# Kernel optimization log

Measured on AMD Instinct MI355X. Metric: run time of the kernel, lower is better.

## Reference

```python
import jax, jax.numpy as jnp
import numpy as np

DIM = 128
HEADS = 4
OUT = DIM // HEADS  # 32
NEG_SLOPE = 0.2
EPS = 1e-16


def setup_inputs() -> dict:
    key = jax.random.key(0)
    k1, k2, k3, k4, k5, k6 = jax.random.split(key, 6)
    B, T, E = 4, 4096, 131072
    x = jax.random.normal(k1, (B, T, DIM), dtype=jnp.float32)
    edge_index = jax.random.randint(k2, (2, E), 0, T, dtype=jnp.int64)
    # GATConv params (PyG layout): lin weight [heads*out, in], att [heads, out], bias [heads*out]
    W = jax.random.normal(k3, (HEADS * OUT, DIM), dtype=jnp.float32) / np.sqrt(DIM)
    att_src = jax.random.normal(k4, (HEADS, OUT), dtype=jnp.float32) / np.sqrt(OUT)
    att_dst = jax.random.normal(k5, (HEADS, OUT), dtype=jnp.float32) / np.sqrt(OUT)
    bias = jax.random.normal(k6, (HEADS * OUT,), dtype=jnp.float32) * 0.01
    return {"x": x, "edge_index": edge_index, "W": W, "att_src": att_src, "att_dst": att_dst, "bias": bias}


def reference(x, edge_index, W, att_src, att_dst, bias):
    B, T, D = x.shape
    N = B * T
    E = edge_index.shape[1]
    # batch the temporal edge list: repeat(1, B) + per-graph node offset b*T
    offsets = jnp.repeat(jnp.arange(B, dtype=edge_index.dtype) * T, E)
    src = jnp.tile(edge_index[0], B) + offsets
    dst = jnp.tile(edge_index[1], B) + offsets
    # PyG GATConv default add_self_loops=True
    loops = jnp.arange(N, dtype=edge_index.dtype)
    src = jnp.concatenate([src, loops])
    dst = jnp.concatenate([dst, loops])

    h = (x.reshape(N, D) @ W.T).reshape(N, HEADS, OUT)          # [N,H,O]
    a_src = jnp.einsum('nho,ho->nh', h, att_src)                # [N,H]
    a_dst = jnp.einsum('nho,ho->nh', h, att_dst)

    e = a_src[src] + a_dst[dst]                                  # [Etot,H]
    e = jax.nn.leaky_relu(e, NEG_SLOPE)
    # segment softmax over destination neighborhoods
    m = jax.ops.segment_max(e, dst, num_segments=N)              # [N,H]
    ex = jnp.exp(e - m[dst])
    s = jax.ops.segment_sum(ex, dst, num_segments=N)
    alpha = ex / (s[dst] + EPS)                                  # [Etot,H]

    msg = h[src] * alpha[:, :, None]                             # [Etot,H,O]
    out = jax.ops.segment_sum(msg, dst, num_segments=N)          # [N,H,O]
    out = out.reshape(N, HEADS * OUT) + bias
    return out.reshape(B, T, D)
```

## Files before the change

kernel.cpp:

```cpp
#include <hip/hip_runtime.h>

#define TPG   4096
#define NHEAD 4
#define DIMD  128
#define NEG   0.2f

__device__ __forceinline__ int load_edge(const void* ei, int is64, long idx) {
  if (is64) return (int)((const long long*)ei)[idx];
  return ((const int*)ei)[idx];
}

__device__ __forceinline__ int detect64_block(const unsigned* __restrict__ ei) {
  __shared__ int s64;
  int t = threadIdx.x;
  if (t == 0) s64 = 1;
  __syncthreads();
  if (t < 256) {
    unsigned v = ei[2 * t + 1];
    if (v != 0u) s64 = 0;
  }
  __syncthreads();
  return s64;
}

__global__ __launch_bounds__(256) void k_gemm(
    const float* __restrict__ x, const float* __restrict__ W,
    const float* __restrict__ atts, const float* __restrict__ attd,
    float* __restrict__ h, float* __restrict__ as_n, float* __restrict__ ad_n,
    int* __restrict__ counts, int* __restrict__ done) {
  __shared__ float4 xs4[16][33];
  int t = threadIdx.x;
  if (blockIdx.x < 16) counts[(blockIdx.x << 8) + t] = 0;
  if (blockIdx.x == 16 && t == 0) *done = 0;
  int base = blockIdx.x * 16;
  const float4* x4 = (const float4*)x;
  for (int i = t; i < 512; i += 256) {
    xs4[i >> 5][i & 31] = x4[base * 32 + i];
  }
  __syncthreads();

  int n_sub = t & 15, cgrp = t >> 4;
  int c0 = cgrp * 8;
  const float4* W4 = (const float4*)W;
  float acc[8];
#pragma unroll
  for (int k = 0; k < 8; ++k) acc[k] = 0.f;

  for (int db = 0; db < 32; db += 8) {
    float4 xa[8];
#pragma unroll
    for (int i = 0; i < 8; ++i) xa[i] = xs4[n_sub][db + i];
#pragma unroll
    for (int k = 0; k < 8; ++k) {
      const float4* wr = W4 + (c0 + k) * 32 + db;
      float a = acc[k];
#pragma unroll
      for (int i = 0; i < 8; ++i) {
        float4 w = wr[i];
        a = fmaf(xa[i].x, w.x, a);
        a = fmaf(xa[i].y, w.y, a);
        a = fmaf(xa[i].z, w.z, a);
        a = fmaf(xa[i].w, w.w, a);
      }
      acc[k] = a;
    }
  }

  int n = base + n_sub;
  float4* hp = (float4*)(h + ((size_t)n << 7) + c0);
  hp[0] = make_float4(acc[0], acc[1], acc[2], acc[3]);
  hp[1] = make_float4(acc[4], acc[5], acc[6], acc[7]);

  float ps = 0.f, pd = 0.f;
#pragma unroll
  for (int k = 0; k < 8; ++k) {
    ps = fmaf(acc[k], atts[c0 + k], ps);
    pd = fmaf(acc[k], attd[c0 + k], pd);
  }
  ps += __shfl_xor(ps, 16); ps += __shfl_xor(ps, 32);
  pd += __shfl_xor(pd, 16); pd += __shfl_xor(pd, 32);
  if ((t & 48) == 0) {
    as_n[(n << 2) + (t >> 6)] = ps;
    ad_n[(n << 2) + (t >> 6)] = pd;
  }
}

__global__ __launch_bounds__(256) void k_histscan(
    const void* __restrict__ ei, int* __restrict__ counts,
    int* __restrict__ offs, int* __restrict__ cursor,
    int* __restrict__ done, int E) {
  int is64 = detect64_block((const unsigned*)ei);
  int t = threadIdx.x;
  int e = blockIdx.x * 256 + t;
  if (e < E) {
    int dst = load_edge(ei, is64, (long)E + e);
    atomicAdd(&counts[dst], 1);
  }
  __syncthreads();
  __shared__ int lastFlag;
  if (t == 0) {
    __threadfence();
    int prev = atomicAdd(done, 1);
    lastFlag = (prev == (int)gridDim.x - 1);
  }
  __syncthreads();
  if (!lastFlag) return;

  int v[16]; int sum = 0;
#pragma unroll
  for (int i = 0; i < 16; ++i) { v[i] = atomicAdd(&counts[t * 16 + i], 0); sum += v[i]; }
  int lane = t & 63, w = t >> 6;
  int sc = sum;
#pragma unroll
  for (int off = 1; off < 64; off <<= 1) {
    int o = __shfl_up(sc, off);
    if (lane >= off) sc += o;
  }
  __shared__ int wsum[4];
  if (lane == 63) wsum[w] = sc;
  __syncthreads();
  int wo = 0;
  for (int i = 0; i < w; ++i) wo += wsum[i];
  int a = wo + sc - sum;
#pragma unroll
  for (int i = 0; i < 16; ++i) {
    offs[t * 16 + i] = a; cursor[t * 16 + i] = a; a += v[i];
  }
  if (t == 255) offs[4096] = a;
}

__global__ __launch_bounds__(256) void k_scatter(const void* __restrict__ ei,
                                                 int* __restrict__ cursor,
                                                 int* __restrict__ esrc, int E) {
  int is64 = detect64_block((const unsigned*)ei);
  int e = blockIdx.x * blockDim.x + threadIdx.x;
  if (e >= E) return;
  int src = load_edge(ei, is64, e);
  int dst = load_edge(ei, is64, (long)E + e);
  int pos = atomicAdd(&cursor[dst], 1);
  esrc[pos] = src;
}

__global__ __launch_bounds__(256) void k_aggr(
    const int* __restrict__ offs, const int* __restrict__ esrc,
    const float* __restrict__ h, const float* __restrict__ as_n,
    const float* __restrict__ ad_n, const float* __restrict__ bias,
    float* __restrict__ out) {
  int bid = blockIdx.x;
  int wv = threadIdx.x >> 6;
  int lane = threadIdx.x & 63;
  int xcd = bid & 7, slot = bid >> 3;
  int g = xcd >> 1, pair = xcd & 1;
  int group = (slot << 1) + pair;
  int n = (g << 12) + (group << 1) + (wv >> 1);
  n = __builtin_amdgcn_readfirstlane(n);
  int hpair = wv & 1;
  int tloc = n & (TPG - 1);
  int nodebase = n - tloc;
  int beg = __builtin_amdgcn_readfirstlane(offs[tloc]);
  int end = __builtin_amdgcn_readfirstlane(offs[tloc + 1]);

  int hh = (hpair << 1) + (lane >> 5);
  int ch = (hh << 5) + (lane & 31);
  float adst = ad_n[(n << 2) + hh];

  float m, s, acc;
  {
    float e = as_n[(n << 2) + hh] + adst;
    e = e > 0.f ? e : NEG * e;
    m = e; s = 1.f;
    acc = h[((size_t)n << 7) + ch];
  }

  for (int j0 = beg; j0 < end; j0 += 8) {
    int sgk[8];
#pragma unroll
    for (int k = 0; k < 8; ++k) {
      int j = j0 + k;
      sgk[k] = (j < end) ? (nodebase + esrc[j]) : n;
    }
    float hv[8];
#pragma unroll
    for (int k = 0; k < 8; ++k) hv[k] = h[((size_t)sgk[k] << 7) + ch];
    float ek[8];
#pragma unroll
    for (int k = 0; k < 8; ++k) {
      float e = as_n[(sgk[k] << 2) + hh] + adst;
      e = e > 0.f ? e : NEG * e;
      ek[k] = (j0 + k < end) ? e : -1e30f;
    }
    float bm = fmaxf(fmaxf(fmaxf(ek[0], ek[1]), fmaxf(ek[2], ek[3])),
                     fmaxf(fmaxf(ek[4], ek[5]), fmaxf(ek[6], ek[7])));
    float mn = fmaxf(m, bm);
    float r = __expf(m - mn);
    float ps = 0.f, pa = 0.f;
#pragma unroll
    for (int k = 0; k < 8; ++k) {
      float al = __expf(ek[k] - mn);
      ps += al;
      pa = fmaf(al, hv[k], pa);
    }
    acc = fmaf(acc, r, pa);
    s = fmaf(s, r, ps);
    m = mn;
  }

  float invs = 1.f / (s + 1e-16f);
  out[((size_t)n << 7) + ch] = fmaf(acc, invs, bias[ch]);
}

extern "C" void kernel_launch(void* const* d_in, const int* in_sizes, int n_in,
                              void* d_out, int out_size, void* d_ws, size_t ws_size,
                              hipStream_t stream) {
  const float* x    = (const float*)d_in[0];
  const void*  ei   = d_in[1];
  const float* W    = (const float*)d_in[2];
  const float* atts = (const float*)d_in[3];
  const float* attd = (const float*)d_in[4];
  const float* bias = (const float*)d_in[5];
  float* out = (float*)d_out;

  int N = in_sizes[0] / DIMD;
  int E = in_sizes[1] / 2;

  char* p = (char*)d_ws;
  float* h      = (float*)p; p += (size_t)N * DIMD * 4;
  float* as_n   = (float*)p; p += (size_t)N * NHEAD * 4;
  float* ad_n   = (float*)p; p += (size_t)N * NHEAD * 4;
  int*   counts = (int*)p;   p += (size_t)TPG * 4;
  int*   offs   = (int*)p;   p += (size_t)(TPG + 1) * 4;
  int*   cursor = (int*)p;   p += (size_t)TPG * 4;
  int*   esrc   = (int*)p;   p += (size_t)E * 4;
  int*   done   = (int*)p;   p += 4;

  k_gemm<<<N / 16, 256, 0, stream>>>(x, W, atts, attd, h, as_n, ad_n, counts, done);
  k_histscan<<<(E + 255) / 256, 256, 0, stream>>>(ei, counts, offs, cursor, done, E);
  k_scatter<<<(E + 255) / 256, 256, 0, stream>>>(ei, cursor, esrc, E);
  k_aggr<<<N / 2, 256, 0, stream>>>(offs, esrc, h, as_n, ad_n, bias, out);
}
```

Before: 170.6 us.

## Process one node per wave with float2 loads and double-buffered edge gathers

The aggregation kernel now assigns a whole wave to one destination node, with each lane handling two channels through float2 loads. It drops the XCD-aware node remapping and halves the grid. The edge loop is software-pipelined with two register buffers, so the next batch's indices and feature gathers are issued before the current batch's softmax math. This aims to hide gather latency and halve per-edge index and score loads, at the cost of more registers and a separate tail path for the leftover edges.

```diff
diff --git a/kernel.cpp b/kernel.cpp
--- a/kernel.cpp
+++ b/kernel.cpp
@@ -4,6 +4,7 @@
 #define NHEAD 4
 #define DIMD  128
 #define NEG   0.2f
+#define BSZ   8
 
 __device__ __forceinline__ int load_edge(const void* ei, int is64, long idx) {
   if (is64) return (int)((const long long*)ei)[idx];
@@ -141,72 +142,125 @@
   esrc[pos] = src;
 }
 
+#define IDX(sg, t)                                                        \
+  { _Pragma("unroll") for (int k = 0; k < BSZ; ++k)                       \
+      sg[k] = nodebase + esrc[beg + ((t) << 3) + k]; }
+
+#define VLD(sg, as, hv)                                                   \
+  { _Pragma("unroll") for (int k = 0; k < BSZ; ++k)                       \
+      as[k] = as_n[(sg[k] << 2) + myh];                                   \
+    _Pragma("unroll") for (int k = 0; k < BSZ; ++k)                       \
+      hv[k] = h2[((size_t)sg[k] << 6) + lane]; }
+
+#define MATH(as, hv)                                                      \
+  { float ek[BSZ];                                                        \
+    _Pragma("unroll") for (int k = 0; k < BSZ; ++k) {                     \
+      float e = as[k] + adst; ek[k] = e > 0.f ? e : NEG * e; }            \
+    float bm = ek[0];                                                     \
+    _Pragma("unroll") for (int k = 1; k < BSZ; ++k) bm = fmaxf(bm, ek[k]);\
+    float mn = fmaxf(m, bm);                                              \
+    float r = __expf(m - mn);                                             \
+    float ps = 0.f, px = 0.f, py = 0.f;                                   \
+    _Pragma("unroll") for (int k = 0; k < BSZ; ++k) {                     \
+      float al = __expf(ek[k] - mn);                                      \
+      ps += al;                                                           \
+      px = fmaf(al, hv[k].x, px);                                         \
+      py = fmaf(al, hv[k].y, py);                                         \
+    }                                                                     \
+    acc.x = fmaf(acc.x, r, px);                                           \
+    acc.y = fmaf(acc.y, r, py);                                           \
+    s = fmaf(s, r, ps);                                                   \
+    m = mn; }
+
 __global__ __launch_bounds__(256) void k_aggr(
     const int* __restrict__ offs, const int* __restrict__ esrc,
     const float* __restrict__ h, const float* __restrict__ as_n,
     const float* __restrict__ ad_n, const float* __restrict__ bias,
     float* __restrict__ out) {
-  int bid = blockIdx.x;
-  int wv = threadIdx.x >> 6;
   int lane = threadIdx.x & 63;
-  int xcd = bid & 7, slot = bid >> 3;
-  int g = xcd >> 1, pair = xcd & 1;
-  int group = (slot << 1) + pair;
-  int n = (g << 12) + (group << 1) + (wv >> 1);
-  n = __builtin_amdgcn_readfirstlane(n);
-  int hpair = wv & 1;
+  int n = __builtin_amdgcn_readfirstlane((blockIdx.x << 2) + (threadIdx.x >> 6));
   int tloc = n & (TPG - 1);
   int nodebase = n - tloc;
   int beg = __builtin_amdgcn_readfirstlane(offs[tloc]);
   int end = __builtin_amdgcn_readfirstlane(offs[tloc + 1]);
 
-  int hh = (hpair << 1) + (lane >> 5);
-  int ch = (hh << 5) + (lane & 31);
-  float adst = ad_n[(n << 2) + hh];
-
-  float m, s, acc;
+  int myh = lane >> 4;
+  const float2* __restrict__ h2 = (const float2*)h;
+  float adst = ad_n[(n << 2) + myh];
+
+  float m, s;
+  float2 acc;
   {
-    float e = as_n[(n << 2) + hh] + adst;
+    float e = as_n[(n << 2) + myh] + adst;
     e = e > 0.f ? e : NEG * e;
     m = e; s = 1.f;
-    acc = h[((size_t)n << 7) + ch];
-  }
-
-  for (int j0 = beg; j0 < end; j0 += 8) {
-    int sgk[8];
-#pragma unroll
-    for (int k = 0; k < 8; ++k) {
-      int j = j0 + k;
-      sgk[k] = (j < end) ? (nodebase + esrc[j]) : n;
-    }
-    float hv[8];
-#pragma unroll
-    for (int k = 0; k < 8; ++k) hv[k] = h[((size_t)sgk[k] << 7) + ch];
-    float ek[8];
-#pragma unroll
-    for (int k = 0; k < 8; ++k) {
-      float e = as_n[(sgk[k] << 2) + hh] + adst;
-      e = e > 0.f ? e : NEG * e;
-      ek[k] = (j0 + k < end) ? e : -1e30f;
-    }
-    float bm = fmaxf(fmaxf(fmaxf(ek[0], ek[1]), fmaxf(ek[2], ek[3])),
-                     fmaxf(fmaxf(ek[4], ek[5]), fmaxf(ek[6], ek[7])));
+    acc = h2[((size_t)n << 6) + lane];
+  }
+
+  int F = (end - beg) >> 3;
+  int sgA[BSZ], sgB[BSZ];
+  float asA[BSZ], asB[BSZ];
+  float2 hvA[BSZ], hvB[BSZ];
+
+  if (F > 0) { IDX(sgA, 0); VLD(sgA, asA, hvA); }
+  if (F > 1) { IDX(sgB, 1); }
+  int t = 0;
+  while (t < F) {
+    if (t + 1 < F) VLD(sgB, asB, hvB);
+    if (t + 2 < F) IDX(sgA, t + 2);
+    MATH(asA, hvA);
+    ++t; if (t >= F) break;
+    if (t + 1 < F) VLD(sgA, asA, hvA);
+    if (t + 2 < F) IDX(sgB, t + 2);
+    MATH(asB, hvB);
+    ++t;
+  }
+
+  int jt = beg + (F << 3);
+  if (jt < end) {
+    int sg[BSZ];
+#pragma unroll
+    for (int k = 0; k < BSZ; ++k) {
+      int j = jt + k;
+      sg[k] = (j < end) ? (nodebase + esrc[j]) : n;
+    }
+    float as_[BSZ]; float2 hv[BSZ];
+#pragma unroll
+    for (int k = 0; k < BSZ; ++k) as_[k] = as_n[(sg[k] << 2) + myh];
+#pragma unroll
+    for (int k = 0; k < BSZ; ++k) hv[k] = h2[((size_t)sg[k] << 6) + lane];
+    float ek[BSZ];
+#pragma unroll
+    for (int k = 0; k < BSZ; ++k) {
+      float e = as_[k] + adst; e = e > 0.f ? e : NEG * e;
+      ek[k] = (jt + k < end) ? e : -1e30f;
+    }
+    float bm = ek[0];
+#pragma unroll
+    for (int k = 1; k < BSZ; ++k) bm = fmaxf(bm, ek[k]);
     float mn = fmaxf(m, bm);
     float r = __expf(m - mn);
-    float ps = 0.f, pa = 0.f;
-#pragma unroll
-    for (int k = 0; k < 8; ++k) {
+    float ps = 0.f, px = 0.f, py = 0.f;
+#pragma unroll
+    for (int k = 0; k < BSZ; ++k) {
       float al = __expf(ek[k] - mn);
       ps += al;
-      pa = fmaf(al, hv[k], pa);
-    }
-    acc = fmaf(acc, r, pa);
+      px = fmaf(al, hv[k].x, px);
+      py = fmaf(al, hv[k].y, py);
+    }
+    acc.x = fmaf(acc.x, r, px);
+    acc.y = fmaf(acc.y, r, py);
     s = fmaf(s, r, ps);
     m = mn;
   }
 
   float invs = 1.f / (s + 1e-16f);
-  out[((size_t)n << 7) + ch] = fmaf(acc, invs, bias[ch]);
+  int c = lane << 1;
+  const float2 bi = *(const float2*)(bias + c);
+  float2 o;
+  o.x = fmaf(acc.x, invs, bi.x);
+  o.y = fmaf(acc.y, invs, bi.y);
+  *(float2*)(out + ((size_t)n << 7) + c) = o;
 }
 
 extern "C" void kernel_launch(void* const* d_in, const int* in_sizes, int n_in,
@@ -236,5 +290,5 @@
   k_gemm<<<N / 16, 256, 0, stream>>>(x, W, atts, attd, h, as_n, ad_n, counts, done);
   k_histscan<<<(E + 255) / 256, 256, 0, stream>>>(ei, counts, offs, cursor, done, E);
   k_scatter<<<(E + 255) / 256, 256, 0, stream>>>(ei, cursor, esrc, E);
-  k_aggr<<<N / 2, 256, 0, stream>>>(offs, esrc, h, as_n, ad_n, bias, out);
-}
+  k_aggr<<<N / 4, 256, 0, stream>>>(offs, esrc, h, as_n, ad_n, bias, out);
+}
```

Measured after the change: 158.8 us. 1.07x faster.

## Fuse all GAT stages into one cooperative persistent kernel with grid syncs

Applied to the files above, without the earlier changes.

Replaces the four separate launches (GEMM, histogram+scan, scatter, aggregation) with a single cooperative kernel that uses grid.sync between phases, to remove launch gaps and inter-kernel bubbles. The aggregation now has one wave handle all four heads of a node with float2 loads and loops over multiple nodes per wave. The cost is four grid-wide barriers, a scan done serially in one block, and a fixed grid of about 512 blocks that may underuse the GPU in the memory-bound phases. A fallback to the multi-kernel path is kept if the cooperative launch fails.

```diff
diff --git a/kernel.cpp b/kernel.cpp
--- a/kernel.cpp
+++ b/kernel.cpp
@@ -1,13 +1,21 @@
 #include <hip/hip_runtime.h>
+#include <hip/hip_cooperative_groups.h>
+
+namespace cg = cooperative_groups;
 
 #define TPG   4096
-#define NHEAD 4
 #define DIMD  128
 #define NEG   0.2f
+#define NTHR  256
+#define COOP_BLK 512
 
 __device__ __forceinline__ int load_edge(const void* ei, int is64, long idx) {
   if (is64) return (int)((const long long*)ei)[idx];
   return ((const int*)ei)[idx];
+}
+
+__device__ __forceinline__ int aload(const int* p) {
+  return __hip_atomic_load(p, __ATOMIC_RELAXED, __HIP_MEMORY_SCOPE_AGENT);
 }
 
 __device__ __forceinline__ int detect64_block(const unsigned* __restrict__ ei) {
@@ -15,12 +23,218 @@
   int t = threadIdx.x;
   if (t == 0) s64 = 1;
   __syncthreads();
-  if (t < 256) {
+  {
     unsigned v = ei[2 * t + 1];
     if (v != 0u) s64 = 0;
   }
   __syncthreads();
   return s64;
+}
+
+__device__ __forceinline__ void gemm_tile(
+    int tile, int t, const float* __restrict__ x, const float* __restrict__ W,
+    const float* __restrict__ atts, const float* __restrict__ attd,
+    float* __restrict__ h, float* __restrict__ as_n, float* __restrict__ ad_n,
+    float4 (*xs4)[33]) {
+  const float4* x4 = (const float4*)x;
+  int base = tile * 16;
+  for (int i = t; i < 512; i += 256) xs4[i >> 5][i & 31] = x4[base * 32 + i];
+  __syncthreads();
+
+  int n_sub = t & 15, cgrp = t >> 4;
+  int c0 = cgrp * 8;
+  const float4* W4 = (const float4*)W;
+  float acc[8];
+#pragma unroll
+  for (int k = 0; k < 8; ++k) acc[k] = 0.f;
+  for (int db = 0; db < 32; db += 8) {
+    float4 xa[8];
+#pragma unroll
+    for (int i = 0; i < 8; ++i) xa[i] = xs4[n_sub][db + i];
+#pragma unroll
+    for (int k = 0; k < 8; ++k) {
+      const float4* wr = W4 + (c0 + k) * 32 + db;
+      float a = acc[k];
+#pragma unroll
+      for (int i = 0; i < 8; ++i) {
+        float4 w = wr[i];
+        a = fmaf(xa[i].x, w.x, a);
+        a = fmaf(xa[i].y, w.y, a);
+        a = fmaf(xa[i].z, w.z, a);
+        a = fmaf(xa[i].w, w.w, a);
+      }
+      acc[k] = a;
+    }
+  }
+  int n = base + n_sub;
+  float4* hp = (float4*)(h + ((size_t)n << 7) + c0);
+  hp[0] = make_float4(acc[0], acc[1], acc[2], acc[3]);
+  hp[1] = make_float4(acc[4], acc[5], acc[6], acc[7]);
+
+  float ps = 0.f, pd = 0.f;
+#pragma unroll
+  for (int k = 0; k < 8; ++k) {
+    ps = fmaf(acc[k], atts[c0 + k], ps);
+    pd = fmaf(acc[k], attd[c0 + k], pd);
+  }
+  ps += __shfl_xor(ps, 16); ps += __shfl_xor(ps, 32);
+  pd += __shfl_xor(pd, 16); pd += __shfl_xor(pd, 32);
+  if ((t & 48) == 0) {
+    as_n[(n << 2) + (t >> 6)] = ps;
+    ad_n[(n << 2) + (t >> 6)] = pd;
+  }
+}
+
+__device__ __forceinline__ void aggr_node(
+    int n, int lane, int beg, int end, const int* __restrict__ esrc,
+    const float* __restrict__ h, const float* __restrict__ as_n,
+    const float* __restrict__ ad_n, const float* __restrict__ bias,
+    float* __restrict__ out, int use_aload) {
+  int tloc = n & (TPG - 1);
+  int nodebase = n - tloc;
+  int myh = lane >> 4;
+  const float2* __restrict__ h2 = (const float2*)h;
+  float adst = ad_n[(n << 2) + myh];
+
+  float m, s;
+  float2 acc;
+  {
+    float e = as_n[(n << 2) + myh] + adst;
+    e = e > 0.f ? e : NEG * e;
+    m = e; s = 1.f;
+    acc = h2[((size_t)n << 6) + lane];
+  }
+
+  for (int j0 = beg; j0 < end; j0 += 8) {
+    int sgk[8];
+#pragma unroll
+    for (int k = 0; k < 8; ++k) {
+      int j = j0 + k;
+      int jj = (j < end) ? j : (end - 1);
+      int v = use_aload ? aload(&esrc[jj]) : esrc[jj];
+      sgk[k] = (j < end) ? (nodebase + v) : n;
+    }
+    float ask[8];
+#pragma unroll
+    for (int k = 0; k < 8; ++k) ask[k] = as_n[(sgk[k] << 2) + myh];
+    float2 hv[8];
+#pragma unroll
+    for (int k = 0; k < 8; ++k) hv[k] = h2[((size_t)sgk[k] << 6) + lane];
+    float ek[8];
+#pragma unroll
+    for (int k = 0; k < 8; ++k) {
+      float e = ask[k] + adst;
+      e = e > 0.f ? e : NEG * e;
+      ek[k] = (j0 + k < end) ? e : -1e30f;
+    }
+    float bm = ek[0];
+#pragma unroll
+    for (int k = 1; k < 8; ++k) bm = fmaxf(bm, ek[k]);
+    float mn = fmaxf(m, bm);
+    float r = __expf(m - mn);
+    float ps = 0.f, px = 0.f, py = 0.f;
+#pragma unroll
+    for (int k = 0; k < 8; ++k) {
+      float al = __expf(ek[k] - mn);
+      ps += al;
+      px = fmaf(al, hv[k].x, px);
+      py = fmaf(al, hv[k].y, py);
+    }
+    acc.x = fmaf(acc.x, r, px);
+    acc.y = fmaf(acc.y, r, py);
+    s = fmaf(s, r, ps);
+    m = mn;
+  }
+
+  float invs = 1.f / (s + 1e-16f);
+  int c = lane << 1;
+  const float2 bi = *(const float2*)(bias + c);
+  float2 o;
+  o.x = fmaf(acc.x, invs, bi.x);
+  o.y = fmaf(acc.y, invs, bi.y);
+  *(float2*)(out + ((size_t)n << 7) + c) = o;
+}
+
+__global__ __launch_bounds__(NTHR, 2) void k_fused(
+    const float* __restrict__ x, const void* __restrict__ ei,
+    const float* __restrict__ W, const float* __restrict__ atts,
+    const float* __restrict__ attd, const float* __restrict__ bias,
+    float* __restrict__ out, float* __restrict__ h,
+    float* __restrict__ as_n, float* __restrict__ ad_n,
+    int* __restrict__ counts, int* __restrict__ offs,
+    int* __restrict__ cursor, int* __restrict__ esrc, int E, int N) {
+  cg::grid_group grid = cg::this_grid();
+  __shared__ float4 xs4[16][33];
+  __shared__ int wsum[4];
+  int t = threadIdx.x;
+  int bid = blockIdx.x;
+  int nb = gridDim.x;
+  int is64 = detect64_block((const unsigned*)ei);
+
+  for (int i = bid * NTHR + t; i < TPG; i += nb * NTHR) counts[i] = 0;
+  int ntile = N / 16;
+  for (int tile = bid; tile < ntile; tile += nb) {
+    gemm_tile(tile, t, x, W, atts, attd, h, as_n, ad_n, xs4);
+    __syncthreads();
+  }
+  grid.sync();
+
+  for (int e = bid * NTHR + t; e < E; e += nb * NTHR) {
+    int dst = load_edge(ei, is64, (long)E + e);
+    atomicAdd(&counts[dst], 1);
+  }
+  grid.sync();
+
+  if (bid == 0) {
+    int v[16]; int sum = 0;
+#pragma unroll
+    for (int i = 0; i < 16; ++i) { v[i] = aload(&counts[t * 16 + i]); sum += v[i]; }
+    int lane = t & 63, w = t >> 6;
+    int sc = sum;
+#pragma unroll
+    for (int off = 1; off < 64; off <<= 1) {
+      int o = __shfl_up(sc, off);
+      if (lane >= off) sc += o;
+    }
+    if (lane == 63) wsum[w] = sc;
+    __syncthreads();
+    int wo = 0;
+    for (int i = 0; i < w; ++i) wo += wsum[i];
+    int a = wo + sc - sum;
+#pragma unroll
+    for (int i = 0; i < 16; ++i) {
+      offs[t * 16 + i] = a; cursor[t * 16 + i] = a; a += v[i];
+    }
+    if (t == 255) offs[4096] = a;
+  }
+  grid.sync();
+
+  for (int e = bid * NTHR + t; e < E; e += nb * NTHR) {
+    int src = load_edge(ei, is64, e);
+    int dst = load_edge(ei, is64, (long)E + e);
+    int pos = atomicAdd(&cursor[dst], 1);
+    esrc[pos] = src;
+  }
+  grid.sync();
+
+  {
+    int wv = t >> 6, lane = t & 63;
+    int xcd = bid & 7;
+    int g = xcd >> 1, pairbit = xcd & 1;
+    int lb = ((bid >> 3) << 1) | pairbit;
+    int blocks_per_graph = nb >> 2;
+    int waves_per_graph = blocks_per_graph << 2;
+    int per_wave = TPG / waves_per_graph;
+    int lw = (lb << 2) + wv;
+    int n0 = (g << 12) + lw * per_wave;
+    for (int i = 0; i < per_wave; ++i) {
+      int n = __builtin_amdgcn_readfirstlane(n0 + i);
+      int tloc = n & (TPG - 1);
+      int beg = __builtin_amdgcn_readfirstlane(aload(&offs[tloc]));
+      int end = __builtin_amdgcn_readfirstlane(aload(&offs[tloc + 1]));
+      aggr_node(n, lane, beg, end, esrc, h, as_n, ad_n, bias, out, 1);
+    }
+  }
 }
 
 __global__ __launch_bounds__(256) void k_gemm(
@@ -32,57 +246,7 @@
   int t = threadIdx.x;
   if (blockIdx.x < 16) counts[(blockIdx.x << 8) + t] = 0;
   if (blockIdx.x == 16 && t == 0) *done = 0;
-  int base = blockIdx.x * 16;
-  const float4* x4 = (const float4*)x;
-  for (int i = t; i < 512; i += 256) {
-    xs4[i >> 5][i & 31] = x4[base * 32 + i];
-  }
-  __syncthreads();
-
-  int n_sub = t & 15, cgrp = t >> 4;
-  int c0 = cgrp * 8;
-  const float4* W4 = (const float4*)W;
-  float acc[8];
-#pragma unroll
-  for (int k = 0; k < 8; ++k) acc[k] = 0.f;
-
-  for (int db = 0; db < 32; db += 8) {
-    float4 xa[8];
-#pragma unroll
-    for (int i = 0; i < 8; ++i) xa[i] = xs4[n_sub][db + i];
-#pragma unroll
-    for (int k = 0; k < 8; ++k) {
-      const float4* wr = W4 + (c0 + k) * 32 + db;
-      float a = acc[k];
-#pragma unroll
-      for (int i = 0; i < 8; ++i) {
-        float4 w = wr[i];
-        a = fmaf(xa[i].x, w.x, a);
-        a = fmaf(xa[i].y, w.y, a);
-        a = fmaf(xa[i].z, w.z, a);
-        a = fmaf(xa[i].w, w.w, a);
-      }
-      acc[k] = a;
-    }
-  }
-
-  int n = base + n_sub;
-  float4* hp = (float4*)(h + ((size_t)n << 7) + c0);
-  hp[0] = make_float4(acc[0], acc[1], acc[2], acc[3]);
-  hp[1] = make_float4(acc[4], acc[5], acc[6], acc[7]);
-
-  float ps = 0.f, pd = 0.f;
-#pragma unroll
-  for (int k = 0; k < 8; ++k) {
-    ps = fmaf(acc[k], atts[c0 + k], ps);
-    pd = fmaf(acc[k], attd[c0 + k], pd);
-  }
-  ps += __shfl_xor(ps, 16); ps += __shfl_xor(ps, 32);
-  pd += __shfl_xor(pd, 16); pd += __shfl_xor(pd, 32);
-  if ((t & 48) == 0) {
-    as_n[(n << 2) + (t >> 6)] = ps;
-    ad_n[(n << 2) + (t >> 6)] = pd;
-  }
+  gemm_tile(blockIdx.x, t, x, W, atts, attd, h, as_n, ad_n, xs4);
 }
 
 __global__ __launch_bounds__(256) void k_histscan(
@@ -108,7 +272,7 @@
 
   int v[16]; int sum = 0;
 #pragma unroll
-  for (int i = 0; i < 16; ++i) { v[i] = atomicAdd(&counts[t * 16 + i], 0); sum += v[i]; }
+  for (int i = 0; i < 16; ++i) { v[i] = aload(&counts[t * 16 + i]); sum += v[i]; }
   int lane = t & 63, w = t >> 6;
   int sc = sum;
 #pragma unroll
@@ -146,67 +310,12 @@
     const float* __restrict__ h, const float* __restrict__ as_n,
     const float* __restrict__ ad_n, const float* __restrict__ bias,
     float* __restrict__ out) {
-  int bid = blockIdx.x;
-  int wv = threadIdx.x >> 6;
   int lane = threadIdx.x & 63;
-  int xcd = bid & 7, slot = bid >> 3;
-  int g = xcd >> 1, pair = xcd & 1;
-  int group = (slot << 1) + pair;
-  int n = (g << 12) + (group << 1) + (wv >> 1);
-  n = __builtin_amdgcn_readfirstlane(n);
-  int hpair = wv & 1;
+  int n = __builtin_amdgcn_readfirstlane((blockIdx.x << 2) + (threadIdx.x >> 6));
   int tloc = n & (TPG - 1);
-  int nodebase = n - tloc;
   int beg = __builtin_amdgcn_readfirstlane(offs[tloc]);
   int end = __builtin_amdgcn_readfirstlane(offs[tloc + 1]);
-
-  int hh = (hpair << 1) + (lane >> 5);
-  int ch = (hh << 5) + (lane & 31);
-  float adst = ad_n[(n << 2) + hh];
-
-  float m, s, acc;
-  {
-    float e = as_n[(n << 2) + hh] + adst;
-    e = e > 0.f ? e : NEG * e;
-    m = e; s = 1.f;
-    acc = h[((size_t)n << 7) + ch];
-  }
-
-  for (int j0 = beg; j0 < end; j0 += 8) {
-    int sgk[8];
-#pragma unroll
-    for (int k = 0; k < 8; ++k) {
-      int j = j0 + k;
-      sgk[k] = (j < end) ? (nodebase + esrc[j]) : n;
-    }
-    float hv[8];
-#pragma unroll
-    for (int k = 0; k < 8; ++k) hv[k] = h[((size_t)sgk[k] << 7) + ch];
-    float ek[8];
-#pragma unroll
-    for (int k = 0; k < 8; ++k) {
-      float e = as_n[(sgk[k] << 2) + hh] + adst;
-      e = e > 0.f ? e : NEG * e;
-      ek[k] = (j0 + k < end) ? e : -1e30f;
-    }
-    float bm = fmaxf(fmaxf(fmaxf(ek[0], ek[1]), fmaxf(ek[2], ek[3])),
-                     fmaxf(fmaxf(ek[4], ek[5]), fmaxf(ek[6], ek[7])));
-    float mn = fmaxf(m, bm);
-    float r = __expf(m - mn);
-    float ps = 0.f, pa = 0.f;
-#pragma unroll
-    for (int k = 0; k < 8; ++k) {
-      float al = __expf(ek[k] - mn);
-      ps += al;
-      pa = fmaf(al, hv[k], pa);
-    }
-    acc = fmaf(acc, r, pa);
-    s = fmaf(s, r, ps);
-    m = mn;
-  }
-
-  float invs = 1.f / (s + 1e-16f);
-  out[((size_t)n << 7) + ch] = fmaf(acc, invs, bias[ch]);
+  aggr_node(n, lane, beg, end, esrc, h, as_n, ad_n, bias, out, 0);
 }
 
 extern "C" void kernel_launch(void* const* d_in, const int* in_sizes, int n_in,
@@ -225,16 +334,40 @@
 
   char* p = (char*)d_ws;
   float* h      = (float*)p; p += (size_t)N * DIMD * 4;
-  float* as_n   = (float*)p; p += (size_t)N * NHEAD * 4;
-  float* ad_n   = (float*)p; p += (size_t)N * NHEAD * 4;
+  float* as_n   = (float*)p; p += (size_t)N * 4 * 4;
+  float* ad_n   = (float*)p; p += (size_t)N * 4 * 4;
   int*   counts = (int*)p;   p += (size_t)TPG * 4;
   int*   offs   = (int*)p;   p += (size_t)(TPG + 1) * 4;
   int*   cursor = (int*)p;   p += (size_t)TPG * 4;
   int*   esrc   = (int*)p;   p += (size_t)E * 4;
   int*   done   = (int*)p;   p += 4;
 
+  int maxBpc = 0;
+  hipError_t qerr = hipOccupancyMaxActiveBlocksPerMultiprocessor(
+      &maxBpc, (const void*)k_fused, NTHR, 0);
+  int grid = COOP_BLK;
+  if (qerr == hipSuccess && maxBpc >= 1) {
+    int cap = maxBpc * 256;
+    if (cap < grid) grid = cap & ~7;
+  }
+  bool coop_ok = (grid >= 8);
+
+  if (coop_ok) {
+    void* args[] = {
+      (void*)&x, (void*)&ei, (void*)&W, (void*)&atts, (void*)&attd, (void*)&bias,
+      (void*)&out, (void*)&h, (void*)&as_n, (void*)&ad_n,
+      (void*)&counts, (void*)&offs, (void*)&cursor, (void*)&esrc,
+      (void*)&E, (void*)&N
+    };
+    hipError_t lerr = hipLaunchCooperativeKernel((const void*)k_fused,
+                                                 dim3(grid), dim3(NTHR),
+                                                 args, 0, stream);
+    if (lerr == hipSuccess) return;
+    (void)hipGetLastError();
+  }
+
   k_gemm<<<N / 16, 256, 0, stream>>>(x, W, atts, attd, h, as_n, ad_n, counts, done);
   k_histscan<<<(E + 255) / 256, 256, 0, stream>>>(ei, counts, offs, cursor, done, E);
   k_scatter<<<(E + 255) / 256, 256, 0, stream>>>(ei, cursor, esrc, E);
-  k_aggr<<<N / 2, 256, 0, stream>>>(offs, esrc, h, as_n, ad_n, bias, out);
-}
+  k_aggr<<<N / 4, 256, 0, stream>>>(offs, esrc, h, as_n, ad_n, bias, out);
+}
```

Measured after the change: 445.0 us. 2.61x slower.

## Store projected features as bf16 and process one node per wavefront in aggregation

Applied to the files above, without the earlier changes.

The GEMM now writes the projected features h as bf16 with round-to-nearest-even instead of fp32. This halves the bytes gathered per edge in the aggregation kernel, which is dominated by random neighbour reads. Aggregation is reorganised so each wavefront handles one whole node, with each lane covering two channels from a packed 32-bit load. That halves the number of wavefronts and redundant index and score loads per node. The histogram scan also uses a relaxed atomic load instead of atomicAdd(0). The bf16 storage of h adds rounding error to the output.

```diff
diff --git a/kernel.cpp b/kernel.cpp
--- a/kernel.cpp
+++ b/kernel.cpp
@@ -1,13 +1,16 @@
 #include <hip/hip_runtime.h>
 
 #define TPG   4096
-#define NHEAD 4
 #define DIMD  128
 #define NEG   0.2f
 
 __device__ __forceinline__ int load_edge(const void* ei, int is64, long idx) {
   if (is64) return (int)((const long long*)ei)[idx];
   return ((const int*)ei)[idx];
+}
+
+__device__ __forceinline__ int aload(const int* p) {
+  return __hip_atomic_load(p, __ATOMIC_RELAXED, __HIP_MEMORY_SCOPE_AGENT);
 }
 
 __device__ __forceinline__ int detect64_block(const unsigned* __restrict__ ei) {
@@ -15,7 +18,7 @@
   int t = threadIdx.x;
   if (t == 0) s64 = 1;
   __syncthreads();
-  if (t < 256) {
+  {
     unsigned v = ei[2 * t + 1];
     if (v != 0u) s64 = 0;
   }
@@ -26,17 +29,15 @@
 __global__ __launch_bounds__(256) void k_gemm(
     const float* __restrict__ x, const float* __restrict__ W,
     const float* __restrict__ atts, const float* __restrict__ attd,
-    float* __restrict__ h, float* __restrict__ as_n, float* __restrict__ ad_n,
-    int* __restrict__ counts, int* __restrict__ done) {
+    unsigned short* __restrict__ hbf, float* __restrict__ as_n,
+    float* __restrict__ ad_n, int* __restrict__ counts, int* __restrict__ done) {
   __shared__ float4 xs4[16][33];
   int t = threadIdx.x;
   if (blockIdx.x < 16) counts[(blockIdx.x << 8) + t] = 0;
   if (blockIdx.x == 16 && t == 0) *done = 0;
   int base = blockIdx.x * 16;
   const float4* x4 = (const float4*)x;
-  for (int i = t; i < 512; i += 256) {
-    xs4[i >> 5][i & 31] = x4[base * 32 + i];
-  }
+  for (int i = t; i < 512; i += 256) xs4[i >> 5][i & 31] = x4[base * 32 + i];
   __syncthreads();
 
   int n_sub = t & 15, cgrp = t >> 4;
@@ -67,9 +68,19 @@
   }
 
   int n = base + n_sub;
-  float4* hp = (float4*)(h + ((size_t)n << 7) + c0);
-  hp[0] = make_float4(acc[0], acc[1], acc[2], acc[3]);
-  hp[1] = make_float4(acc[4], acc[5], acc[6], acc[7]);
+  uint4 pk;
+  unsigned r[8];
+#pragma unroll
+  for (int k = 0; k < 8; ++k) {
+    unsigned u = __float_as_uint(acc[k]);
+    unsigned rnd = ((u >> 16) & 1u) + 0x7fffu;
+    r[k] = (u + rnd) >> 16;
+  }
+  pk.x = r[0] | (r[1] << 16);
+  pk.y = r[2] | (r[3] << 16);
+  pk.z = r[4] | (r[5] << 16);
+  pk.w = r[6] | (r[7] << 16);
+  *(uint4*)(hbf + ((size_t)n << 7) + c0) = pk;
 
   float ps = 0.f, pd = 0.f;
 #pragma unroll
@@ -108,7 +119,7 @@
 
   int v[16]; int sum = 0;
 #pragma unroll
-  for (int i = 0; i < 16; ++i) { v[i] = atomicAdd(&counts[t * 16 + i], 0); sum += v[i]; }
+  for (int i = 0; i < 16; ++i) { v[i] = aload(&counts[t * 16 + i]); sum += v[i]; }
   int lane = t & 63, w = t >> 6;
   int sc = sum;
 #pragma unroll
@@ -143,33 +154,33 @@
 
 __global__ __launch_bounds__(256) void k_aggr(
     const int* __restrict__ offs, const int* __restrict__ esrc,
-    const float* __restrict__ h, const float* __restrict__ as_n,
+    const unsigned* __restrict__ h2, const float* __restrict__ as_n,
     const float* __restrict__ ad_n, const float* __restrict__ bias,
     float* __restrict__ out) {
   int bid = blockIdx.x;
   int wv = threadIdx.x >> 6;
   int lane = threadIdx.x & 63;
-  int xcd = bid & 7, slot = bid >> 3;
-  int g = xcd >> 1, pair = xcd & 1;
-  int group = (slot << 1) + pair;
-  int n = (g << 12) + (group << 1) + (wv >> 1);
-  n = __builtin_amdgcn_readfirstlane(n);
-  int hpair = wv & 1;
+  int xcd = bid & 7;
+  int g = xcd >> 1;
+  int lb = ((bid >> 3) << 1) | (xcd & 1);
+  int nodebase = g << 12;
+  int n = __builtin_amdgcn_readfirstlane(nodebase + (lb << 2) + wv);
   int tloc = n & (TPG - 1);
-  int nodebase = n - tloc;
   int beg = __builtin_amdgcn_readfirstlane(offs[tloc]);
   int end = __builtin_amdgcn_readfirstlane(offs[tloc + 1]);
 
-  int hh = (hpair << 1) + (lane >> 5);
-  int ch = (hh << 5) + (lane & 31);
-  float adst = ad_n[(n << 2) + hh];
-
-  float m, s, acc;
+  int myh = lane >> 4;
+  float adst = ad_n[(n << 2) + myh];
+
+  float m, s;
+  float ax, ay;
   {
-    float e = as_n[(n << 2) + hh] + adst;
+    float e = as_n[(n << 2) + myh] + adst;
     e = e > 0.f ? e : NEG * e;
     m = e; s = 1.f;
-    acc = h[((size_t)n << 7) + ch];
+    unsigned v = h2[((size_t)n << 6) + lane];
+    ax = __uint_as_float(v << 16);
+    ay = __uint_as_float(v & 0xffff0000u);
   }
 
   for (int j0 = beg; j0 < end; j0 += 8) {
@@ -179,13 +190,16 @@
       int j = j0 + k;
       sgk[k] = (j < end) ? (nodebase + esrc[j]) : n;
     }
-    float hv[8];
-#pragma unroll
-    for (int k = 0; k < 8; ++k) hv[k] = h[((size_t)sgk[k] << 7) + ch];
+    unsigned hv[8];
+#pragma unroll
+    for (int k = 0; k < 8; ++k) hv[k] = h2[((size_t)sgk[k] << 6) + lane];
+    float ask[8];
+#pragma unroll
+    for (int k = 0; k < 8; ++k) ask[k] = as_n[(sgk[k] << 2) + myh];
     float ek[8];
 #pragma unroll
     for (int k = 0; k < 8; ++k) {
-      float e = as_n[(sgk[k] << 2) + hh] + adst;
+      float e = ask[k] + adst;
       e = e > 0.f ? e : NEG * e;
       ek[k] = (j0 + k < end) ? e : -1e30f;
     }
@@ -193,20 +207,27 @@
                      fmaxf(fmaxf(ek[4], ek[5]), fmaxf(ek[6], ek[7])));
     float mn = fmaxf(m, bm);
     float r = __expf(m - mn);
-    float ps = 0.f, pa = 0.f;
+    float ps = 0.f, px = 0.f, py = 0.f;
 #pragma unroll
     for (int k = 0; k < 8; ++k) {
       float al = __expf(ek[k] - mn);
       ps += al;
-      pa = fmaf(al, hv[k], pa);
-    }
-    acc = fmaf(acc, r, pa);
+      px = fmaf(al, __uint_as_float(hv[k] << 16), px);
+      py = fmaf(al, __uint_as_float(hv[k] & 0xffff0000u), py);
+    }
+    ax = fmaf(ax, r, px);
+    ay = fmaf(ay, r, py);
     s = fmaf(s, r, ps);
     m = mn;
   }
 
   float invs = 1.f / (s + 1e-16f);
-  out[((size_t)n << 7) + ch] = fmaf(acc, invs, bias[ch]);
+  int c = lane << 1;
+  const float2 bi = *(const float2*)(bias + c);
+  float2 o;
+  o.x = fmaf(ax, invs, bi.x);
+  o.y = fmaf(ay, invs, bi.y);
+  *(float2*)(out + ((size_t)n << 7) + c) = o;
 }
 
 extern "C" void kernel_launch(void* const* d_in, const int* in_sizes, int n_in,
@@ -224,17 +245,17 @@
   int E = in_sizes[1] / 2;
 
   char* p = (char*)d_ws;
-  float* h      = (float*)p; p += (size_t)N * DIMD * 4;
-  float* as_n   = (float*)p; p += (size_t)N * NHEAD * 4;
-  float* ad_n   = (float*)p; p += (size_t)N * NHEAD * 4;
+  unsigned short* hbf = (unsigned short*)p; p += (size_t)N * DIMD * 2;
+  float* as_n   = (float*)p; p += (size_t)N * 4 * 4;
+  float* ad_n   = (float*)p; p += (size_t)N * 4 * 4;
   int*   counts = (int*)p;   p += (size_t)TPG * 4;
   int*   offs   = (int*)p;   p += (size_t)(TPG + 1) * 4;
   int*   cursor = (int*)p;   p += (size_t)TPG * 4;
   int*   esrc   = (int*)p;   p += (size_t)E * 4;
   int*   done   = (int*)p;   p += 4;
 
-  k_gemm<<<N / 16, 256, 0, stream>>>(x, W, atts, attd, h, as_n, ad_n, counts, done);
+  k_gemm<<<N / 16, 256, 0, stream>>>(x, W, atts, attd, hbf, as_n, ad_n, counts, done);
   k_histscan<<<(E + 255) / 256, 256, 0, stream>>>(ei, counts, offs, cursor, done, E);
   k_scatter<<<(E + 255) / 256, 256, 0, stream>>>(ei, cursor, esrc, E);
-  k_aggr<<<N / 2, 256, 0, stream>>>(offs, esrc, h, as_n, ad_n, bias, out);
-}
+  k_aggr<<<N / 4, 256, 0, stream>>>(offs, esrc, (const unsigned*)hbf, as_n, ad_n, bias, out);
+}
```

After: 155.6 us. -8.8%, faster.
